# Kernel tuning notes

Measured on AMD Instinct MI355X. Metric: run time of the kernel, lower is better.

The kernel has to match this reference:

```python
import jax, jax.numpy as jnp
import numpy as np

KERNEL = 25  # moving_avg


def _series_decomp_trend(x, kernel):
    # x: [B, L, N]; replicate-pad ends then moving average over time (AvgPool1d stride 1)
    pad = (kernel - 1) // 2
    front = jnp.repeat(x[:, :1, :], pad, axis=1)
    end = jnp.repeat(x[:, -1:, :], pad, axis=1)
    xp = jnp.concatenate([front, x, end], axis=1)  # [B, L+2*pad, N]
    cs = jnp.cumsum(xp, axis=1)
    cs = jnp.concatenate([jnp.zeros_like(cs[:, :1, :]), cs], axis=1)
    trend = (cs[:, kernel:, :] - cs[:, :-kernel, :]) / kernel  # [B, L, N]
    return trend


def setup_inputs() -> dict:
    key = jax.random.key(0)
    k1, k2, k3 = jax.random.split(key, 3)
    B, L, N = 128, 512, 321
    x_enc = jax.random.normal(k1, (B, L, N), dtype=jnp.float32)
    W_trend = jax.random.normal(k2, (L, L), dtype=jnp.float32) * (1.0 / L)
    b_trend = jax.random.normal(k3, (L,), dtype=jnp.float32) * 0.02
    return {"x_enc": x_enc, "W_trend": W_trend, "b_trend": b_trend}


def reference(x_enc, W_trend, b_trend):
    B, L, N = x_enc.shape
    # series_decomp: only the trend branch is consumed downstream
    trend = _series_decomp_trend(x_enc, KERNEL)          # [B, L, N]
    trend_init = trend.transpose(0, 2, 1)                # [B, N, L]
    # Linear_Trend: seq_len -> pred_len (== L)
    trend_out = jnp.einsum('bnl,pl->bnp', trend_init, W_trend) + b_trend  # [B, N, L]
    # closed-form OLS per (b, n): X_b = [1, t] for t in [-L, 0)
    t_old = jnp.arange(-L, 0, dtype=jnp.float32)
    t_new = jnp.arange(L, dtype=jnp.float32)
    X_b = jnp.stack([jnp.ones(L, jnp.float32), t_old], axis=1)      # [L, 2]
    X_new_b = jnp.stack([jnp.ones(L, jnp.float32), t_new], axis=1)  # [L, 2]
    XTX = X_b.T @ X_b                                    # [2, 2]
    XTy = jnp.einsum('lt,bnl->bnt', X_b, trend_out)      # [B, N, 2]
    inv = jnp.linalg.inv(XTX)                            # symmetric 2x2
    theta = jnp.einsum('bnt,ts->bns', XTy, inv)          # [B, N, 2]
    pred = jnp.einsum('pt,bnt->bnp', X_new_b, theta)     # [B, N, L]
    out = pred.transpose(0, 2, 1)                        # [B, L, N]
    return out[:, -L:, :]  # pred_len == L, so this is the full output
```

## Files before the change

kernel.cpp:

```cpp
#include <hip/hip_runtime.h>

#define LSEQ 512
#define NCH  321
#define BATCH 128
#define KAVG 25
#define PAD  12
#define NB1A 8
#define ROWS1A 64

#define BANDS 4
#define BROWS 128
#define ITERS 64
#define RTHREADS 704

#define ROWS_W 32
#define WBLOCKS (LSEQ / ROWS_W)
#define CHUNKW  (ROWS_W * NCH)

typedef float f32x4 __attribute__((ext_vector_type(4)));

constexpr double S1d  = -131328.0;
constexpr double S2d  = 44870400.0;
constexpr double DETD = 512.0 * S2d - S1d * S1d;
constexpr double I00  = S2d / DETD;
constexpr double I01  = -S1d / DETD;
constexpr double I11  = 512.0 / DETD;

__global__ __launch_bounds__(512) void colsum_kernel(const float* __restrict__ W,
                                                     float* __restrict__ part0,
                                                     float* __restrict__ part1) {
    int l = threadIdx.x;
    int p0 = blockIdx.x * ROWS1A;
    double s0 = 0.0, s1 = 0.0;
#pragma unroll
    for (int r = 0; r < ROWS1A; ++r) {
        float w = W[(p0 + r) * LSEQ + l];
        s0 += (double)w;
        s1 += (double)(p0 + r - LSEQ) * (double)w;
    }
    part0[blockIdx.x * LSEQ + l] = (float)s0;
    part1[blockIdx.x * LSEQ + l] = (float)s1;
}

__global__ __launch_bounds__(RTHREADS) void reduce_kernel(const float* __restrict__ x,
                                                          const float* __restrict__ part0,
                                                          const float* __restrict__ part1,
                                                          const float* __restrict__ bvec,
                                                          float* __restrict__ P0,
                                                          float* __restrict__ P1) {
    __shared__ double w0d[LSEQ], w1d[LSEQ];
    __shared__ double r0[LSEQ], r1[LSEQ];
    __shared__ float la[LSEQ], lbb[LSEQ];
    __shared__ float cbuf0[NCH], cbuf1[NCH];
    __shared__ float cc0, cc1;

    int tid = threadIdx.x;

    if (tid < LSEQ) {
        int l = tid;
        double s0 = 0.0, s1 = 0.0;
#pragma unroll
        for (int j = 0; j < NB1A; ++j) {
            s0 += (double)part0[j * LSEQ + l];
            s1 += (double)part1[j * LSEQ + l];
        }
        w0d[l] = s0;
        w1d[l] = s1;
        double bv = (double)bvec[l];
        r0[l] = bv;
        r1[l] = (double)(l - LSEQ) * bv;
    }
    __syncthreads();
    if (tid < LSEQ) {
        int l = tid;
        double g0 = 0.0, g1 = 0.0;
        for (int m = l - PAD; m <= l + PAD; ++m) {
            if (m >= 0 && m < LSEQ) { g0 += w0d[m]; g1 += w1d[m]; }
        }
        if (l == 0) {
            for (int m = 0; m < PAD; ++m) {
                double c = (double)(PAD - m);
                g0 += c * w0d[m]; g1 += c * w1d[m];
            }
        }
        if (l == LSEQ - 1) {
            for (int m = LSEQ - PAD; m < LSEQ; ++m) {
                double c = (double)(m - (LSEQ - PAD - 1));
                g0 += c * w0d[m]; g1 += c * w1d[m];
            }
        }
        g0 *= (1.0 / (double)KAVG);
        g1 *= (1.0 / (double)KAVG);
        la[l]  = (float)(I00 * g0 + I01 * g1);
        lbb[l] = (float)(I01 * g0 + I11 * g1);
    }
    for (int s = LSEQ / 2; s > 0; s >>= 1) {
        __syncthreads();
        if (tid < s) { r0[tid] += r0[tid + s]; r1[tid] += r1[tid + s]; }
    }
    if (tid == 0) {
        cc0 = (float)(I00 * r0[0] + I01 * r1[0]);
        cc1 = (float)(I01 * r0[0] + I11 * r1[0]);
    }
    __syncthreads();

    int band = blockIdx.x;
    int b    = blockIdx.y;
    int half = (tid >= NCH) ? 1 : 0;
    int n    = tid - half * NCH;
    bool act = (tid < 2 * NCH);
    int l0   = band * BROWS;

    float a = 0.f, bb = 0.f;
    if (act) {
        const float* xp = x + (size_t)b * (LSEQ * NCH) + (size_t)l0 * NCH + tid;
#pragma unroll 8
        for (int it = 0; it < ITERS; ++it) {
            float v = xp[it * (2 * NCH)];
            int l = l0 + 2 * it + half;
            a  = fmaf(v, la[l],  a);
            bb = fmaf(v, lbb[l], bb);
        }
    }

    if (act && half == 0) { cbuf0[n] = a; cbuf1[n] = bb; }
    __syncthreads();
    if (act && half == 1) { cbuf0[n] += a; cbuf1[n] += bb; }
    __syncthreads();

    if (tid < NCH) {
        float add0 = (band == 0) ? cc0 : 0.f;
        float add1 = (band == 0) ? cc1 : 0.f;
        P0[(band * BATCH + b) * NCH + tid] = cbuf0[tid] + add0;
        P1[(band * BATCH + b) * NCH + tid] = cbuf1[tid] + add1;
    }
}

__global__ __launch_bounds__(256) void write_kernel(const float* __restrict__ P0,
                                                    const float* __restrict__ P1,
                                                    float* __restrict__ out) {
    __shared__ float t0s[NCH], t1s[NCH];
    int tid = threadIdx.x;
    int b = blockIdx.y;
    for (int i = tid; i < NCH; i += 256) {
        float s0 = 0.f, s1 = 0.f;
#pragma unroll
        for (int band = 0; band < BANDS; ++band) {
            s0 += P0[(band * BATCH + b) * NCH + i];
            s1 += P1[(band * BATCH + b) * NCH + i];
        }
        t0s[i] = s0;
        t1s[i] = s1;
    }
    __syncthreads();

    int pbase = blockIdx.x * ROWS_W;
    float* op = out + (size_t)b * (LSEQ * NCH) + (size_t)pbase * NCH;
    for (int g = tid; g < CHUNKW / 4; g += 256) {
        int c0 = 4 * g;
        int ploc = c0 / NCH;
        int n = c0 - ploc * NCH;
        float pf = (float)(pbase + ploc);
        f32x4 v;
        v.x = fmaf(pf, t1s[n], t0s[n]); if (++n == NCH) { n = 0; pf += 1.f; }
        v.y = fmaf(pf, t1s[n], t0s[n]); if (++n == NCH) { n = 0; pf += 1.f; }
        v.z = fmaf(pf, t1s[n], t0s[n]); if (++n == NCH) { n = 0; pf += 1.f; }
        v.w = fmaf(pf, t1s[n], t0s[n]);
        __builtin_nontemporal_store(v, reinterpret_cast<f32x4*>(op + c0));
    }
}

extern "C" void kernel_launch(void* const* d_in, const int* in_sizes, int n_in,
                              void* d_out, int out_size, void* d_ws, size_t ws_size,
                              hipStream_t stream) {
    (void)in_sizes; (void)n_in; (void)out_size; (void)ws_size;
    const float* x    = (const float*)d_in[0];
    const float* W    = (const float*)d_in[1];
    const float* bvec = (const float*)d_in[2];
    float* out = (float*)d_out;

    float* p0 = (float*)d_ws;
    float* p1 = p0 + NB1A * LSEQ;
    float* P0 = p1 + NB1A * LSEQ;
    float* P1 = P0 + BANDS * BATCH * NCH;

    colsum_kernel<<<NB1A, LSEQ, 0, stream>>>(W, p0, p1);
    reduce_kernel<<<dim3(BANDS, BATCH), RTHREADS, 0, stream>>>(x, p0, p1, bvec, P0, P1);
    write_kernel<<<dim3(WBLOCKS, BATCH), 256, 0, stream>>>(P0, P1, out);
}
```

Before: 42.52 us.

## Fuse three kernels into one cooperative kernel with grid-wide syncs

Replaces the colsum, reduce and write launches with a single cooperative kernel of 256 blocks that uses grid syncs between the W column-sum phase, the x reduction phase and the output write phase. It also halves the band count, so each block reduces 256 rows instead of 128. The aim is to cut launch gaps and the inter-kernel tail effects. In exchange it adds two grid-wide barriers and lower parallelism in the write phase. It falls back to the old three-kernel path if the cooperative launch fails.

Result: slower. 96.63 us (+127.2%).

```diff
diff --git a/kernel.cpp b/kernel.cpp
--- a/kernel.cpp
+++ b/kernel.cpp
@@ -1,4 +1,7 @@
 #include <hip/hip_runtime.h>
+#include <hip/hip_cooperative_groups.h>
+
+namespace cg = cooperative_groups;
 
 #define LSEQ 512
 #define NCH  321
@@ -8,11 +11,17 @@
 #define NB1A 8
 #define ROWS1A 64
 
+#define RTHREADS 704
+
+#define FBANDS 2
+#define FBROWS 256
+#define FITERS 128
+#define FNBLOCKS (FBANDS * BATCH)
+#define FWCHUNK (FBROWS * NCH)
+
 #define BANDS 4
 #define BROWS 128
 #define ITERS 64
-#define RTHREADS 704
-
 #define ROWS_W 32
 #define WBLOCKS (LSEQ / ROWS_W)
 #define CHUNKW  (ROWS_W * NCH)
@@ -25,6 +34,152 @@
 constexpr double I00  = S2d / DETD;
 constexpr double I01  = -S1d / DETD;
 constexpr double I11  = 512.0 / DETD;
+
+__device__ __forceinline__ void prep_in_lds(const float* __restrict__ part0,
+                                            const float* __restrict__ part1,
+                                            const float* __restrict__ bvec,
+                                            double* w0d, double* w1d,
+                                            double* r0, double* r1,
+                                            float* la, float* lbb,
+                                            float* cc, int tid) {
+    if (tid < LSEQ) {
+        int l = tid;
+        double s0 = 0.0, s1 = 0.0;
+#pragma unroll
+        for (int j = 0; j < NB1A; ++j) {
+            s0 += (double)part0[j * LSEQ + l];
+            s1 += (double)part1[j * LSEQ + l];
+        }
+        w0d[l] = s0;
+        w1d[l] = s1;
+        double bv = (double)bvec[l];
+        r0[l] = bv;
+        r1[l] = (double)(l - LSEQ) * bv;
+    }
+    __syncthreads();
+    if (tid < LSEQ) {
+        int l = tid;
+        double g0 = 0.0, g1 = 0.0;
+        for (int m = l - PAD; m <= l + PAD; ++m) {
+            if (m >= 0 && m < LSEQ) { g0 += w0d[m]; g1 += w1d[m]; }
+        }
+        if (l == 0) {
+            for (int m = 0; m < PAD; ++m) {
+                double c = (double)(PAD - m);
+                g0 += c * w0d[m]; g1 += c * w1d[m];
+            }
+        }
+        if (l == LSEQ - 1) {
+            for (int m = LSEQ - PAD; m < LSEQ; ++m) {
+                double c = (double)(m - (LSEQ - PAD - 1));
+                g0 += c * w0d[m]; g1 += c * w1d[m];
+            }
+        }
+        g0 *= (1.0 / (double)KAVG);
+        g1 *= (1.0 / (double)KAVG);
+        la[l]  = (float)(I00 * g0 + I01 * g1);
+        lbb[l] = (float)(I01 * g0 + I11 * g1);
+    }
+    for (int s = LSEQ / 2; s > 0; s >>= 1) {
+        __syncthreads();
+        if (tid < s) { r0[tid] += r0[tid + s]; r1[tid] += r1[tid + s]; }
+    }
+    if (tid == 0) {
+        cc[0] = (float)(I00 * r0[0] + I01 * r1[0]);
+        cc[1] = (float)(I01 * r0[0] + I11 * r1[0]);
+    }
+    __syncthreads();
+}
+
+__global__ __launch_bounds__(RTHREADS, 3) void fused_kernel(
+        const float* __restrict__ x, const float* __restrict__ W,
+        const float* __restrict__ bvec,
+        float* __restrict__ part0, float* __restrict__ part1,
+        float* __restrict__ P0, float* __restrict__ P1,
+        float* __restrict__ out) {
+    __shared__ double w0d[LSEQ], w1d[LSEQ];
+    __shared__ double r0[LSEQ], r1[LSEQ];
+    __shared__ float la[LSEQ], lbb[LSEQ];
+    __shared__ float cbuf0[NCH], cbuf1[NCH];
+    __shared__ float cc[2];
+
+    int tid  = threadIdx.x;
+    int bid  = blockIdx.x;
+    int band = bid >> 7;
+    int b    = bid & 127;
+
+    if (bid < NB1A && tid < LSEQ) {
+        int l = tid;
+        int p0r = bid * ROWS1A;
+        double s0 = 0.0, s1 = 0.0;
+#pragma unroll
+        for (int r = 0; r < ROWS1A; ++r) {
+            float w = W[(p0r + r) * LSEQ + l];
+            s0 += (double)w;
+            s1 += (double)(p0r + r - LSEQ) * (double)w;
+        }
+        part0[bid * LSEQ + l] = (float)s0;
+        part1[bid * LSEQ + l] = (float)s1;
+    }
+    cg::this_grid().sync();
+
+    prep_in_lds(part0, part1, bvec, w0d, w1d, r0, r1, la, lbb, cc, tid);
+
+    int half = (tid >= NCH) ? 1 : 0;
+    int n    = tid - half * NCH;
+    bool act = (tid < 2 * NCH);
+    int l0   = band * FBROWS;
+
+    float a = 0.f, bb = 0.f;
+    if (act) {
+        const float* xp = x + (size_t)b * (LSEQ * NCH) + (size_t)l0 * NCH + tid;
+#pragma unroll 8
+        for (int it = 0; it < FITERS; ++it) {
+            float v = xp[it * (2 * NCH)];
+            int l = l0 + 2 * it + half;
+            a  = fmaf(v, la[l],  a);
+            bb = fmaf(v, lbb[l], bb);
+        }
+    }
+    if (act && half == 0) { cbuf0[n] = a; cbuf1[n] = bb; }
+    __syncthreads();
+    if (act && half == 1) { cbuf0[n] += a; cbuf1[n] += bb; }
+    __syncthreads();
+    if (tid < NCH) {
+        float add0 = (band == 0) ? cc[0] : 0.f;
+        float add1 = (band == 0) ? cc[1] : 0.f;
+        P0[(band * BATCH + b) * NCH + tid] = cbuf0[tid] + add0;
+        P1[(band * BATCH + b) * NCH + tid] = cbuf1[tid] + add1;
+    }
+    cg::this_grid().sync();
+
+    for (int i = tid; i < NCH; i += RTHREADS) {
+        float s0 = 0.f, s1 = 0.f;
+#pragma unroll
+        for (int bd = 0; bd < FBANDS; ++bd) {
+            s0 += P0[(bd * BATCH + b) * NCH + i];
+            s1 += P1[(bd * BATCH + b) * NCH + i];
+        }
+        cbuf0[i] = s0;
+        cbuf1[i] = s1;
+    }
+    __syncthreads();
+
+    int pbase = band * FBROWS;
+    float* op = out + (size_t)b * (LSEQ * NCH) + (size_t)pbase * NCH;
+    for (int g = tid; g < FWCHUNK / 4; g += RTHREADS) {
+        int c0 = 4 * g;
+        int ploc = c0 / NCH;
+        int nn = c0 - ploc * NCH;
+        float pf = (float)(pbase + ploc);
+        f32x4 v;
+        v.x = fmaf(pf, cbuf1[nn], cbuf0[nn]); if (++nn == NCH) { nn = 0; pf += 1.f; }
+        v.y = fmaf(pf, cbuf1[nn], cbuf0[nn]); if (++nn == NCH) { nn = 0; pf += 1.f; }
+        v.z = fmaf(pf, cbuf1[nn], cbuf0[nn]); if (++nn == NCH) { nn = 0; pf += 1.f; }
+        v.w = fmaf(pf, cbuf1[nn], cbuf0[nn]);
+        __builtin_nontemporal_store(v, reinterpret_cast<f32x4*>(op + c0));
+    }
+}
 
 __global__ __launch_bounds__(512) void colsum_kernel(const float* __restrict__ W,
                                                      float* __restrict__ part0,
@@ -52,57 +207,9 @@
     __shared__ double r0[LSEQ], r1[LSEQ];
     __shared__ float la[LSEQ], lbb[LSEQ];
     __shared__ float cbuf0[NCH], cbuf1[NCH];
-    __shared__ float cc0, cc1;
-
+    __shared__ float cc[2];
     int tid = threadIdx.x;
-
-    if (tid < LSEQ) {
-        int l = tid;
-        double s0 = 0.0, s1 = 0.0;
-#pragma unroll
-        for (int j = 0; j < NB1A; ++j) {
-            s0 += (double)part0[j * LSEQ + l];
-            s1 += (double)part1[j * LSEQ + l];
-        }
-        w0d[l] = s0;
-        w1d[l] = s1;
-        double bv = (double)bvec[l];
-        r0[l] = bv;
-        r1[l] = (double)(l - LSEQ) * bv;
-    }
-    __syncthreads();
-    if (tid < LSEQ) {
-        int l = tid;
-        double g0 = 0.0, g1 = 0.0;
-        for (int m = l - PAD; m <= l + PAD; ++m) {
-            if (m >= 0 && m < LSEQ) { g0 += w0d[m]; g1 += w1d[m]; }
-        }
-        if (l == 0) {
-            for (int m = 0; m < PAD; ++m) {
-                double c = (double)(PAD - m);
-                g0 += c * w0d[m]; g1 += c * w1d[m];
-            }
-        }
-        if (l == LSEQ - 1) {
-            for (int m = LSEQ - PAD; m < LSEQ; ++m) {
-                double c = (double)(m - (LSEQ - PAD - 1));
-                g0 += c * w0d[m]; g1 += c * w1d[m];
-            }
-        }
-        g0 *= (1.0 / (double)KAVG);
-        g1 *= (1.0 / (double)KAVG);
-        la[l]  = (float)(I00 * g0 + I01 * g1);
-        lbb[l] = (float)(I01 * g0 + I11 * g1);
-    }
-    for (int s = LSEQ / 2; s > 0; s >>= 1) {
-        __syncthreads();
-        if (tid < s) { r0[tid] += r0[tid + s]; r1[tid] += r1[tid + s]; }
-    }
-    if (tid == 0) {
-        cc0 = (float)(I00 * r0[0] + I01 * r1[0]);
-        cc1 = (float)(I01 * r0[0] + I11 * r1[0]);
-    }
-    __syncthreads();
+    prep_in_lds(part0, part1, bvec, w0d, w1d, r0, r1, la, lbb, cc, tid);
 
     int band = blockIdx.x;
     int b    = blockIdx.y;
@@ -122,15 +229,13 @@
             bb = fmaf(v, lbb[l], bb);
         }
     }
-
     if (act && half == 0) { cbuf0[n] = a; cbuf1[n] = bb; }
     __syncthreads();
     if (act && half == 1) { cbuf0[n] += a; cbuf1[n] += bb; }
     __syncthreads();
-
     if (tid < NCH) {
-        float add0 = (band == 0) ? cc0 : 0.f;
-        float add1 = (band == 0) ? cc1 : 0.f;
+        float add0 = (band == 0) ? cc[0] : 0.f;
+        float add1 = (band == 0) ? cc[1] : 0.f;
         P0[(band * BATCH + b) * NCH + tid] = cbuf0[tid] + add0;
         P1[(band * BATCH + b) * NCH + tid] = cbuf1[tid] + add1;
     }
@@ -184,7 +289,15 @@
     float* P0 = p1 + NB1A * LSEQ;
     float* P1 = P0 + BANDS * BATCH * NCH;
 
-    colsum_kernel<<<NB1A, LSEQ, 0, stream>>>(W, p0, p1);
-    reduce_kernel<<<dim3(BANDS, BATCH), RTHREADS, 0, stream>>>(x, p0, p1, bvec, P0, P1);
-    write_kernel<<<dim3(WBLOCKS, BATCH), 256, 0, stream>>>(P0, P1, out);
-}
+    void* args[] = { (void*)&x, (void*)&W, (void*)&bvec,
+                     (void*)&p0, (void*)&p1, (void*)&P0, (void*)&P1,
+                     (void*)&out };
+    hipError_t err = hipLaunchCooperativeKernel(
+        reinterpret_cast<void*>(fused_kernel),
+        dim3(FNBLOCKS), dim3(RTHREADS), args, 0, stream);
+    if (err != hipSuccess) {
+        colsum_kernel<<<NB1A, LSEQ, 0, stream>>>(W, p0, p1);
+        reduce_kernel<<<dim3(BANDS, BATCH), RTHREADS, 0, stream>>>(x, p0, p1, bvec, P0, P1);
+        write_kernel<<<dim3(WBLOCKS, BATCH), 256, 0, stream>>>(P0, P1, out);
+    }
+}
```
